# Optimization experiments

Measured on AMD Instinct MI355X. Metric: run time of the kernel, lower is better.

## Reference

```python
import jax, jax.numpy as jnp
import numpy as np
import math

B, N, D, H = 32, 512, 512, 8
DK = D // H
MAX_DIST = 100.0
BINS = 20
BIN_SIZE = MAX_DIST / BINS


def setup_inputs() -> dict:
    key = jax.random.key(0)
    ks = jax.random.split(key, 12)
    s = 1.0 / math.sqrt(D)
    inp = {
        "x": jax.random.normal(ks[0], (B, N, D), dtype=jnp.float32),
        "distance_matrix": jax.random.uniform(ks[1], (B, N, N), dtype=jnp.float32) * MAX_DIST,
        "Wq": jax.random.uniform(ks[2], (D, D), jnp.float32, -s, s),
        "bq": jax.random.uniform(ks[3], (D,), jnp.float32, -s, s),
        "Wk": jax.random.uniform(ks[4], (D, D), jnp.float32, -s, s),
        "bk": jax.random.uniform(ks[5], (D,), jnp.float32, -s, s),
        "Wv": jax.random.uniform(ks[6], (D, D), jnp.float32, -s, s),
        "bv": jax.random.uniform(ks[7], (D,), jnp.float32, -s, s),
        "Wo": jax.random.uniform(ks[8], (D, D), jnp.float32, -s, s),
        "bo": jax.random.uniform(ks[9], (D,), jnp.float32, -s, s),
        "dist_weights": jnp.ones((BINS + 1,), dtype=jnp.float32),
    }
    return inp


def reference(x, distance_matrix, Wq, bq, Wk, bk, Wv, bv, Wo, bo, dist_weights):
    temperature = 1.0
    # Linear projections; torch nn.Linear computes x @ W.T + b
    q = (x @ Wq.T + bq).reshape(B, N, H, DK).transpose(0, 2, 1, 3)  # [B,H,N,DK]
    k = (x @ Wk.T + bk).reshape(B, N, H, DK).transpose(0, 2, 1, 3)
    v = (x @ Wv.T + bv).reshape(B, N, H, DK).transpose(0, 2, 1, 3)

    scores = jnp.einsum("bhqd,bhkd->bhqk", q, k) / math.sqrt(DK)  # [B,H,N,N]

    # Relative position bias: bin distances, look up scalar weight per pair
    binned = jnp.clip((distance_matrix / BIN_SIZE).astype(jnp.int32), 0, BINS)  # [B,N,N]
    bias = dist_weights[binned] / temperature  # [B,N,N]
    scores = scores + bias[:, None, :, :]  # broadcast over heads

    attn = jax.nn.softmax(scores, axis=-1)  # dropout is identity in eval
    out = jnp.einsum("bhqk,bhkd->bhqd", attn, v)  # [B,H,N,DK]
    out = out.transpose(0, 2, 1, 3).reshape(B, N, D)
    return out @ Wo.T + bo
```

## Files before the change

kernel.cpp:

```cpp
#include <hip/hip_runtime.h>
#include <hip/hip_fp16.h>
#include <math.h>
#include <stdint.h>

#define BB 32
#define NN 512
#define DDIM 512
#define HH 8
#define DK 64

typedef __attribute__((ext_vector_type(8))) short short8;
typedef __attribute__((ext_vector_type(8))) _Float16 half8;
typedef __attribute__((ext_vector_type(4))) float floatx4;
typedef __attribute__((ext_vector_type(16))) float floatx16;
typedef unsigned short ushort_t;
typedef unsigned int uint_t;

__device__ __forceinline__ void gl_lds16(const void* g, void* l) {
    __builtin_amdgcn_global_load_lds(
        (const __attribute__((address_space(1))) uint_t*)g,
        (__attribute__((address_space(3))) uint_t*)l,
        16, 0, 0);
}

__device__ __forceinline__ ushort_t f2bf(float f) {
    uint_t u = __builtin_bit_cast(uint_t, f);
    u += 0x7fff + ((u >> 16) & 1);
    return (ushort_t)(u >> 16);
}

__device__ __forceinline__ uint_t pkbf(float a, float b) {
    return (uint_t)f2bf(a) | ((uint_t)f2bf(b) << 16);
}

__device__ __forceinline__ uint_t pkh(float a, float b) {
    return __builtin_bit_cast(uint_t, __builtin_amdgcn_cvt_pkrtz(a, b));
}

__device__ __forceinline__ float h2f(ushort_t u) {
    return __half2float(__ushort_as_half(u));
}

__global__ __launch_bounds__(256) void prep_all(
    const float* __restrict__ x, const float* __restrict__ dist,
    const float* __restrict__ dw,
    const float* __restrict__ Wq, const float* __restrict__ Wk,
    const float* __restrict__ Wv, const float* __restrict__ Wo,
    ushort_t* __restrict__ xb, ushort_t* __restrict__ Tm,
    ushort_t* __restrict__ wqb, ushort_t* __restrict__ wkb,
    ushort_t* __restrict__ wvb, ushort_t* __restrict__ wob) {
    const int bx = blockIdx.x;
    if (bx < 4096) {
        const int i = bx * 256 + threadIdx.x;
        const float4 a = ((const float4*)x)[i * 2 + 0];
        const float4 b = ((const float4*)x)[i * 2 + 1];
        uint4 o;
        o.x = pkbf(a.x, a.y); o.y = pkbf(a.z, a.w);
        o.z = pkbf(b.x, b.y); o.w = pkbf(b.z, b.w);
        *(uint4*)(xb + (size_t)i * 8) = o;
    } else if (bx < 8192) {
        __shared__ float dws[21];
        if (threadIdx.x < 21) dws[threadIdx.x] = (dw[threadIdx.x] - 3.0f) * 1.44269504f;
        __syncthreads();
        const int i = (bx - 4096) * 256 + threadIdx.x;
        float dv[8];
        { const float4 a = ((const float4*)dist)[i * 2 + 0];
          const float4 b = ((const float4*)dist)[i * 2 + 1];
          dv[0]=a.x; dv[1]=a.y; dv[2]=a.z; dv[3]=a.w;
          dv[4]=b.x; dv[5]=b.y; dv[6]=b.z; dv[7]=b.w; }
        ushort_t h[8];
        #pragma unroll
        for (int j = 0; j < 8; ++j) {
            int bin = (int)(dv[j] / 5.0f);
            bin = bin < 0 ? 0 : (bin > 20 ? 20 : bin);
            h[j] = __half_as_ushort(__float2half(dws[bin]));
        }
        uint4 o;
        o.x = (uint_t)h[0] | ((uint_t)h[1] << 16);
        o.y = (uint_t)h[2] | ((uint_t)h[3] << 16);
        o.z = (uint_t)h[4] | ((uint_t)h[5] << 16);
        o.w = (uint_t)h[6] | ((uint_t)h[7] << 16);
        *(uint4*)(Tm + (size_t)i * 8) = o;
    } else {
        const int bw = bx - 8192;
        const int w = bw >> 7;
        const float* s; ushort_t* d;
        if (w == 0)      { s = Wq; d = wqb; }
        else if (w == 1) { s = Wk; d = wkb; }
        else if (w == 2) { s = Wv; d = wvb; }
        else             { s = Wo; d = wob; }
        const int i = (bw & 127) * 256 + threadIdx.x;
        const float4 a = ((const float4*)s)[i * 2 + 0];
        const float4 b = ((const float4*)s)[i * 2 + 1];
        uint4 o;
        o.x = pkbf(a.x, a.y); o.y = pkbf(a.z, a.w);
        o.z = pkbf(b.x, b.y); o.w = pkbf(b.z, b.w);
        *(uint4*)(d + (size_t)i * 8) = o;
    }
}

#define GEMM_CORE(Aptr, Wptr, M0, N0)                                                   \
    __shared__ ushort_t SH[2][128 * 32];                                                \
    ushort_t* const As = SH[0];                                                         \
    ushort_t* const Bs = SH[1];                                                         \
    const int tid = threadIdx.x;                                                        \
    const int lane = tid & 63, wid = tid >> 6;                                          \
    const int quad = lane >> 4, l15 = lane & 15;                                        \
    const int m0 = (M0), n0 = (N0);                                                     \
    const int wy = wid >> 1, wx = wid & 1;                                              \
    floatx4 acc[4][4];                                                                  \
    _Pragma("unroll") for (int i = 0; i < 4; ++i)                                       \
        _Pragma("unroll") for (int j = 0; j < 4; ++j)                                   \
            _Pragma("unroll") for (int r = 0; r < 4; ++r) acc[i][j][r] = 0.f;           \
    for (int k0 = 0; k0 < DDIM; k0 += 32) {                                             \
        __syncthreads();                                                                \
        _Pragma("unroll") for (int j = 0; j < 4; ++j) {                                 \
            const int t = wid * 4 + j;                                                  \
            const int rowi = ((t & 7) << 4) + (lane >> 2);                              \
            const int cd = (lane & 3) ^ ((rowi >> 1) & 3);                              \
            if (t < 8)                                                                  \
                gl_lds16(Aptr + (size_t)(m0 + rowi) * DDIM + k0 + cd * 8,               \
                         (char*)As + ((t & 7) << 10));                                  \
            else                                                                        \
                gl_lds16(Wptr + (size_t)(n0 + rowi) * DDIM + k0 + cd * 8,               \
                         (char*)Bs + ((t & 7) << 10));                                  \
        }                                                                               \
        __syncthreads();                                                                \
        short8 aw[4], bt[4];                                                            \
        _Pragma("unroll") for (int fi = 0; fi < 4; ++fi) {                              \
            const int r = wy * 64 + fi * 16 + l15;                                      \
            aw[fi] = *(const short8*)((const char*)Bs + r * 64 +                        \
                                      ((quad ^ ((r >> 1) & 3)) << 4));                  \
        }                                                                               \
        _Pragma("unroll") for (int ti = 0; ti < 4; ++ti) {                              \
            const int r = wx * 64 + ti * 16 + l15;                                      \
            bt[ti] = *(const short8*)((const char*)As + r * 64 +                        \
                                      ((quad ^ ((r >> 1) & 3)) << 4));                  \
        }                                                                               \
        _Pragma("unroll") for (int fi = 0; fi < 4; ++fi)                                \
            _Pragma("unroll") for (int ti = 0; ti < 4; ++ti)                            \
                acc[fi][ti] = __builtin_amdgcn_mfma_f32_16x16x32_bf16(                  \
                    aw[fi], bt[ti], acc[fi][ti], 0, 0, 0);                              \
    }

__global__ __launch_bounds__(256)
__attribute__((amdgpu_waves_per_eu(2, 2)))
void gemm_qkv(
    const ushort_t* __restrict__ A,
    const ushort_t* __restrict__ W0, const ushort_t* __restrict__ W1,
    const ushort_t* __restrict__ W2,
    const float* __restrict__ b0, const float* __restrict__ b1,
    const float* __restrict__ b2,
    ushort_t* __restrict__ o0, ushort_t* __restrict__ o1, ushort_t* __restrict__ o2) {
    __shared__ ushort_t SH[4][128 * 32];
    const int tid = threadIdx.x;
    const int lane = tid & 63, wid = tid >> 6;
    const int quad = lane >> 4, l15 = lane & 15;
    const int m0 = blockIdx.x * 128, n0 = blockIdx.y * 128;
    const int wy = wid >> 1, wx = wid & 1;

    floatx4 acc[3][4][4];
    #pragma unroll
    for (int w = 0; w < 3; ++w)
        #pragma unroll
        for (int i = 0; i < 4; ++i)
            #pragma unroll
            for (int j = 0; j < 4; ++j)
                #pragma unroll
                for (int r = 0; r < 4; ++r) acc[w][i][j][r] = 0.f;

    const ushort_t* const stage_src =
        (wid == 0) ? A : (wid == 1 ? W0 : (wid == 2 ? W1 : W2));
    const int stage_base = (wid == 0) ? m0 : n0;

    for (int k0 = 0; k0 < DDIM; k0 += 32) {
        __syncthreads();
        #pragma unroll
        for (int j = 0; j < 8; ++j) {
            const int rowi = (j << 4) + (lane >> 2);
            const int cd = (lane & 3) ^ ((rowi >> 1) & 3);
            gl_lds16(stage_src + (size_t)(stage_base + rowi) * DDIM + k0 + cd * 8,
                     (char*)&SH[wid][0] + (j << 10));
        }
        __syncthreads();
        short8 bt[4];
        #pragma unroll
        for (int ti = 0; ti < 4; ++ti) {
            const int r = wx * 64 + ti * 16 + l15;
            bt[ti] = *(const short8*)((const char*)&SH[0][0] + r * 64 +
                                      ((quad ^ ((r >> 1) & 3)) << 4));
        }
        #pragma unroll
        for (int w = 0; w < 3; ++w) {
            short8 aw[4];
            #pragma unroll
            for (int fi = 0; fi < 4; ++fi) {
                const int r = wy * 64 + fi * 16 + l15;
                aw[fi] = *(const short8*)((const char*)&SH[1 + w][0] + r * 64 +
                                          ((quad ^ ((r >> 1) & 3)) << 4));
            }
            #pragma unroll
            for (int fi = 0; fi < 4; ++fi)
                #pragma unroll
                for (int ti = 0; ti < 4; ++ti)
                    acc[w][fi][ti] = __builtin_amdgcn_mfma_f32_16x16x32_bf16(
                        aw[fi], bt[ti], acc[w][fi][ti], 0, 0, 0);
        }
    }

    #pragma unroll
    for (int w = 0; w < 2; ++w) {
        const float* const bias = w ? b1 : b0;
        ushort_t* const dst = w ? o1 : o0;
        #pragma unroll
        for (int fi = 0; fi < 4; ++fi) {
            const int f = n0 + wy * 64 + fi * 16 + quad * 4;
            const float4 b4 = *(const float4*)&bias[f];
            #pragma unroll
            for (int ti = 0; ti < 4; ++ti) {
                const int token = m0 + wx * 64 + ti * 16 + l15;
                const float v0 = acc[w][fi][ti][0] + b4.x, v1 = acc[w][fi][ti][1] + b4.y;
                const float v2 = acc[w][fi][ti][2] + b4.z, v3 = acc[w][fi][ti][3] + b4.w;
                uint2 v;
                v.x = pkbf(v0, v1); v.y = pkbf(v2, v3);
                *(uint2*)&dst[(size_t)token * DDIM + f] = v;
            }
        }
    }

    {
        const int b = m0 >> 9;
        const int hh0 = n0 >> 6;
        ushort_t* const SHT = &SH[0][0];
        __syncthreads();
        #pragma unroll
        for (int hp = 0; hp < 2; ++hp) {
            if (wy == hp) {
                #pragma unroll
                for (int fi = 0; fi < 4; ++fi) {
                    const int f = n0 + wy * 64 + fi * 16 + quad * 4;
                    const float4 b4 = *(const float4*)&b2[f];
                    #pragma unroll
                    for (int ti = 0; ti < 4; ++ti) {
                        const int q = wx * 64 + ti * 16 + l15;
                        const int qc = q >> 3, qr = q & 7;
                        const float vv[4] = {acc[2][fi][ti][0] + b4.x,
                                             acc[2][fi][ti][1] + b4.y,
                                             acc[2][fi][ti][2] + b4.z,
                                             acc[2][fi][ti][3] + b4.w};
                        #pragma unroll
                        for (int r = 0; r < 4; ++r) {
                            const int d = fi * 16 + quad * 4 + r;
                            SHT[(d * 256 + ((qc ^ (d & 15)) << 4) + qr * 2) >> 1] =
                                __half_as_ushort(__float2half(vv[r]));
                        }
                    }
                }
            }
            __syncthreads();
            const size_t vbase = ((size_t)(b * HH + hh0 + hp)) * DK;
            #pragma unroll
            for (int c = 0; c < 4; ++c) {
                const int ch = tid + 256 * c;
                const int d = ch >> 4, chl = ch & 15;
                const uint4 vv = *(const uint4*)((const char*)SHT + d * 256 +
                                                 ((chl ^ (d & 15)) << 4));
                *(uint4*)&o2[(vbase + d) * NN + (m0 & 511) + chl * 8] = vv;
            }
            __syncthreads();
        }
    }
}

__global__ __launch_bounds__(256) void gemm_out(
    const ushort_t* __restrict__ A, const ushort_t* __restrict__ Wo,
    const float* __restrict__ bo, float* __restrict__ dst) {
    GEMM_CORE(A, Wo, blockIdx.x * 128, blockIdx.y * 128)
    #pragma unroll
    for (int fi = 0; fi < 4; ++fi) {
        const int f = n0 + wy * 64 + fi * 16 + quad * 4;
        const float4 b4 = *(const float4*)&bo[f];
        #pragma unroll
        for (int ti = 0; ti < 4; ++ti) {
            const int token = m0 + wx * 64 + ti * 16 + l15;
            float4 v;
            v.x = acc[fi][ti][0] + b4.x; v.y = acc[fi][ti][1] + b4.y;
            v.z = acc[fi][ti][2] + b4.z; v.w = acc[fi][ti][3] + b4.w;
            *(float4*)&dst[(size_t)token * DDIM + f] = v;
        }
    }
}

__global__ __launch_bounds__(512)
__attribute__((amdgpu_waves_per_eu(2, 2)))
void attn_fused(
    const ushort_t* __restrict__ Qg, const ushort_t* __restrict__ Kg,
    const ushort_t* __restrict__ Vtg, const ushort_t* __restrict__ Tg,
    ushort_t* __restrict__ aout) {
    __shared__ ushort_t Ks[512 * 64];
    __shared__ ushort_t Vs[64 * 512];

    const int tid = threadIdx.x, lane = tid & 63, wid = tid >> 6;
    const int l31 = lane & 31, hl = lane >> 5;
    const int p = blockIdx.x;
    const int nid = (p & 7) * 32 + (p >> 3);
    const int h = nid & 7, b = nid >> 3;
    const float K1 = 0.18033688f;

    #pragma unroll
    for (int j = 0; j < 8; ++j) {
        const int t = wid * 8 + j;
        {
            const int row = t * 8 + (lane >> 3);
            const int key = (row & 7) ^ ((row >> 3) & 7);
            const int g = (lane & 7) ^ key;
            gl_lds16(Kg + (size_t)(b * NN + row) * DDIM + h * DK + g * 8,
                     (char*)Ks + t * 1024);
        }
        {
            const int key = (t & 7) ^ ((t >> 3) & 7);
            const int g = lane ^ key;
            gl_lds16(Vtg + (size_t)((b * HH + h) * DK + t) * NN + g * 8,
                     (char*)Vs + t * 1024);
        }
    }

    short8 bq[2][4];
    #pragma unroll
    for (int qt = 0; qt < 2; ++qt) {
        const ushort_t* qp =
            Qg + (size_t)(b * NN + wid * 64 + qt * 32 + l31) * DDIM + h * DK + hl * 8;
        #pragma unroll
        for (int st = 0; st < 4; ++st) bq[qt][st] = *(const short8*)(qp + st * 16);
    }

    float lsum[2] = {0.f, 0.f};
    floatx16 O[2][2];
    #pragma unroll
    for (int qt = 0; qt < 2; ++qt)
        #pragma unroll
        for (int dt = 0; dt < 2; ++dt)
            #pragma unroll
            for (int r = 0; r < 16; ++r) O[qt][dt][r] = 0.f;

    __syncthreads();

    for (int kt = 0; kt < 8; ++kt) {
        uint2 tv[2][2][4];
        #pragma unroll
        for (int qt = 0; qt < 2; ++qt) {
            const ushort_t* tp =
                Tg + (size_t)(b * NN + wid * 64 + qt * 32 + l31) * NN + kt * 64 + hl * 4;
            #pragma unroll
            for (int kti = 0; kti < 2; ++kti)
                #pragma unroll
                for (int g = 0; g < 4; ++g)
                    tv[qt][kti][g] = *(const uint2*)(tp + kti * 32 + g * 8);
        }

        #pragma unroll
        for (int kti = 0; kti < 2; ++kti) {
            short8 kf[4];
            {
                const int row = kt * 64 + kti * 32 + l31;
                const int key = (row & 7) ^ ((row >> 3) & 7);
                #pragma unroll
                for (int st = 0; st < 4; ++st)
                    kf[st] = *(const short8*)((const char*)Ks + row * 128 +
                                              (((st * 2 + hl) ^ key) << 4));
            }
            half8 vf[2][2];
            #pragma unroll
            for (int dt = 0; dt < 2; ++dt) {
                const int d = dt * 32 + l31;
                const int key = (d & 7) ^ ((d >> 3) & 7);
                #pragma unroll
                for (int ks = 0; ks < 2; ++ks)
                    vf[dt][ks] = *(const half8*)((const char*)Vs + d * 1024 +
                        (((kt * 8 + kti * 4 + ks * 2 + hl) ^ key) << 4));
            }

            #pragma unroll
            for (int qt = 0; qt < 2; ++qt) {
                floatx16 S;
                #pragma unroll
                for (int r = 0; r < 16; ++r) S[r] = 0.f;
                __builtin_amdgcn_s_setprio(1);
                #pragma unroll
                for (int st = 0; st < 4; ++st)
                    S = __builtin_amdgcn_mfma_f32_32x32x16_bf16(
                        kf[st], bq[qt][st], S, 0, 0, 0);
                __builtin_amdgcn_s_setprio(0);

                float ls = 0.f;
                #pragma unroll
                for (int ks = 0; ks < 2; ++ks) {
                    float pp[8];
                    #pragma unroll
                    for (int gg = 0; gg < 2; ++gg) {
                        const uint2 tg = tv[qt][kti][ks * 2 + gg];
                        const float t0 = h2f((ushort_t)tg.x);
                        const float t1 = h2f((ushort_t)(tg.x >> 16));
                        const float t2 = h2f((ushort_t)tg.y);
                        const float t3 = h2f((ushort_t)(tg.y >> 16));
                        const int sb = ks * 8 + gg * 4;
                        pp[gg * 4 + 0] = exp2f(S[sb + 0] * K1 + t0);
                        pp[gg * 4 + 1] = exp2f(S[sb + 1] * K1 + t1);
                        pp[gg * 4 + 2] = exp2f(S[sb + 2] * K1 + t2);
                        pp[gg * 4 + 3] = exp2f(S[sb + 3] * K1 + t3);
                        ls += (pp[gg * 4 + 0] + pp[gg * 4 + 1]) +
                              (pp[gg * 4 + 2] + pp[gg * 4 + 3]);
                    }
                    uint_t w0 = pkh(pp[0], pp[1]);
                    uint_t w1 = pkh(pp[2], pp[3]);
                    uint_t w2 = pkh(pp[4], pp[5]);
                    uint_t w3 = pkh(pp[6], pp[7]);
                    auto r02 = __builtin_amdgcn_permlane32_swap(w0, w2, false, false);
                    auto r13 = __builtin_amdgcn_permlane32_swap(w1, w3, false, false);
                    uint4 uu;
                    uu.x = r02[0];
                    uu.y = r13[0];
                    uu.z = r02[1];
                    uu.w = r13[1];
                    const half8 bp = __builtin_bit_cast(half8, uu);

                    __builtin_amdgcn_s_setprio(1);
                    #pragma unroll
                    for (int dt = 0; dt < 2; ++dt)
                        O[qt][dt] = __builtin_amdgcn_mfma_f32_32x32x16_f16(
                            vf[dt][ks], bp, O[qt][dt], 0, 0, 0);
                    __builtin_amdgcn_s_setprio(0);
                }
                lsum[qt] += ls;
            }
        }
    }

    #pragma unroll
    for (int qt = 0; qt < 2; ++qt) {
        float l = lsum[qt];
        l += __shfl_xor(l, 32);
        const float inv = 1.0f / l;
        const size_t orow =
            (size_t)(b * NN + wid * 64 + qt * 32 + l31) * DDIM + h * DK;
        #pragma unroll
        for (int dt = 0; dt < 2; ++dt)
            #pragma unroll
            for (int g = 0; g < 4; ++g) {
                const int d = dt * 32 + g * 8 + hl * 4;
                uint2 ov;
                ov.x = pkbf(O[qt][dt][g * 4 + 0] * inv, O[qt][dt][g * 4 + 1] * inv);
                ov.y = pkbf(O[qt][dt][g * 4 + 2] * inv, O[qt][dt][g * 4 + 3] * inv);
                *(uint2*)&aout[orow + d] = ov;
            }
    }
}

extern "C" void kernel_launch(void* const* d_in, const int* in_sizes, int n_in,
                              void* d_out, int out_size, void* d_ws, size_t ws_size,
                              hipStream_t stream) {
    const float* x    = (const float*)d_in[0];
    const float* dist = (const float*)d_in[1];
    const float* Wq   = (const float*)d_in[2];
    const float* bq   = (const float*)d_in[3];
    const float* Wk   = (const float*)d_in[4];
    const float* bk   = (const float*)d_in[5];
    const float* Wv   = (const float*)d_in[6];
    const float* bv   = (const float*)d_in[7];
    const float* Wo   = (const float*)d_in[8];
    const float* bo   = (const float*)d_in[9];
    const float* dw   = (const float*)d_in[10];
    float* out = (float*)d_out;

    const size_t NELT = (size_t)BB * NN * DDIM;
    ushort_t* xb  = (ushort_t*)d_ws;
    ushort_t* wqb = xb + NELT;
    ushort_t* wkb = wqb + DDIM * DDIM;
    ushort_t* wvb = wkb + DDIM * DDIM;
    ushort_t* wob = wvb + DDIM * DDIM;
    ushort_t* qb  = wob + DDIM * DDIM;
    ushort_t* kb  = qb + NELT;
    ushort_t* vt  = kb + NELT;
    ushort_t* Tm  = vt + NELT;
    ushort_t* ab  = xb;

    prep_all<<<8704, 256, 0, stream>>>(x, dist, dw, Wq, Wk, Wv, Wo,
                                       xb, Tm, wqb, wkb, wvb, wob);
    gemm_qkv<<<dim3(128, 4), 256, 0, stream>>>(xb, wqb, wkb, wvb, bq, bk, bv,
                                               qb, kb, vt);
    attn_fused<<<256, 512, 0, stream>>>(qb, kb, vt, Tm, ab);
    gemm_out<<<dim3(128, 4), 256, 0, stream>>>(ab, wob, bo, out);
}
```

Before: 224.9 us.

## Split attention blocks over query halves, read V fragments from global in MFMA layout

The attention kernel now launches twice as many blocks, each handling half the query rows of a (batch, head), with one 32-row query tile per wave instead of two. The V tile is no longer staged in LDS. The QKV GEMM now writes V^T in a 16-query chunked layout so each lane can load its MFMA fragment straight from global/L2, and the occupancy hint rises to 4 waves per EU. This is meant to cut LDS use and per-block register pressure to raise occupancy on the 256 CUs. In exchange, V is re-read from L2 by every wave and K is loaded into LDS twice per (batch, head).

```diff
diff --git a/kernel.cpp b/kernel.cpp
--- a/kernel.cpp
+++ b/kernel.cpp
@@ -231,6 +231,7 @@
     {
         const int b = m0 >> 9;
         const int hh0 = n0 >> 6;
+        const int q0 = m0 & 511;
         ushort_t* const SHT = &SH[0][0];
         __syncthreads();
         #pragma unroll
@@ -258,14 +259,15 @@
                 }
             }
             __syncthreads();
-            const size_t vbase = ((size_t)(b * HH + hh0 + hp)) * DK;
+            const size_t slab = (size_t)(b * HH + hh0 + hp) * DK * NN;
             #pragma unroll
             for (int c = 0; c < 4; ++c) {
-                const int ch = tid + 256 * c;
-                const int d = ch >> 4, chl = ch & 15;
+                const int idx = c * 256 + tid;
+                const int d = (idx >> 1) & 63, hf = idx & 1, qc2 = idx >> 7;
+                const int qchl = qc2 * 2 + hf;
                 const uint4 vv = *(const uint4*)((const char*)SHT + d * 256 +
-                                                 ((chl ^ (d & 15)) << 4));
-                *(uint4*)&o2[(vbase + d) * NN + (m0 & 511) + chl * 8] = vv;
+                                                 ((qchl ^ (d & 15)) << 4));
+                *(uint4*)&o2[slab + (size_t)((q0 >> 4) + qc2) * 1024 + d * 16 + hf * 8] = vv;
             }
             __syncthreads();
         }
@@ -292,74 +294,73 @@
 }
 
 __global__ __launch_bounds__(512)
-__attribute__((amdgpu_waves_per_eu(2, 2)))
+__attribute__((amdgpu_waves_per_eu(4, 4)))
 void attn_fused(
     const ushort_t* __restrict__ Qg, const ushort_t* __restrict__ Kg,
     const ushort_t* __restrict__ Vtg, const ushort_t* __restrict__ Tg,
     ushort_t* __restrict__ aout) {
     __shared__ ushort_t Ks[512 * 64];
-    __shared__ ushort_t Vs[64 * 512];
 
     const int tid = threadIdx.x, lane = tid & 63, wid = tid >> 6;
     const int l31 = lane & 31, hl = lane >> 5;
     const int p = blockIdx.x;
-    const int nid = (p & 7) * 32 + (p >> 3);
-    const int h = nid & 7, b = nid >> 3;
+    const int nid = (p & 7) * 64 + (p >> 3);
+    const int h = nid & 7, b = (nid >> 3) & 31, qh = nid >> 8;
+    const int qbase = qh * 256 + wid * 32;
     const float K1 = 0.18033688f;
 
     #pragma unroll
     for (int j = 0; j < 8; ++j) {
         const int t = wid * 8 + j;
+        const int row = t * 8 + (lane >> 3);
+        const int key = (row & 7) ^ ((row >> 3) & 7);
+        const int g = (lane & 7) ^ key;
+        gl_lds16(Kg + (size_t)(b * NN + row) * DDIM + h * DK + g * 8,
+                 (char*)Ks + t * 1024);
+    }
+
+    short8 bq[4];
+    {
+        const ushort_t* qp =
+            Qg + (size_t)(b * NN + qbase + l31) * DDIM + h * DK + hl * 8;
+        #pragma unroll
+        for (int st = 0; st < 4; ++st) bq[st] = *(const short8*)(qp + st * 16);
+    }
+
+    const ushort_t* const vslab = Vtg + (size_t)(b * HH + h) * DK * NN;
+
+    float lsum = 0.f;
+    floatx16 O[2];
+    #pragma unroll
+    for (int dt = 0; dt < 2; ++dt)
+        #pragma unroll
+        for (int r = 0; r < 16; ++r) O[dt][r] = 0.f;
+
+    __syncthreads();
+
+    for (int kt = 0; kt < 8; ++kt) {
+        uint2 tv[2][4];
         {
-            const int row = t * 8 + (lane >> 3);
-            const int key = (row & 7) ^ ((row >> 3) & 7);
-            const int g = (lane & 7) ^ key;
-            gl_lds16(Kg + (size_t)(b * NN + row) * DDIM + h * DK + g * 8,
-                     (char*)Ks + t * 1024);
-        }
-        {
-            const int key = (t & 7) ^ ((t >> 3) & 7);
-            const int g = lane ^ key;
-            gl_lds16(Vtg + (size_t)((b * HH + h) * DK + t) * NN + g * 8,
-                     (char*)Vs + t * 1024);
-        }
-    }
-
-    short8 bq[2][4];
-    #pragma unroll
-    for (int qt = 0; qt < 2; ++qt) {
-        const ushort_t* qp =
-            Qg + (size_t)(b * NN + wid * 64 + qt * 32 + l31) * DDIM + h * DK + hl * 8;
-        #pragma unroll
-        for (int st = 0; st < 4; ++st) bq[qt][st] = *(const short8*)(qp + st * 16);
-    }
-
-    float lsum[2] = {0.f, 0.f};
-    floatx16 O[2][2];
-    #pragma unroll
-    for (int qt = 0; qt < 2; ++qt)
-        #pragma unroll
-        for (int dt = 0; dt < 2; ++dt)
-            #pragma unroll
-            for (int r = 0; r < 16; ++r) O[qt][dt][r] = 0.f;
-
-    __syncthreads();
-
-    for (int kt = 0; kt < 8; ++kt) {
-        uint2 tv[2][2][4];
-        #pragma unroll
-        for (int qt = 0; qt < 2; ++qt) {
             const ushort_t* tp =
-                Tg + (size_t)(b * NN + wid * 64 + qt * 32 + l31) * NN + kt * 64 + hl * 4;
+                Tg + (size_t)(b * NN + qbase + l31) * NN + kt * 64 + hl * 4;
             #pragma unroll
             for (int kti = 0; kti < 2; ++kti)
                 #pragma unroll
                 for (int g = 0; g < 4; ++g)
-                    tv[qt][kti][g] = *(const uint2*)(tp + kti * 32 + g * 8);
+                    tv[kti][g] = *(const uint2*)(tp + kti * 32 + g * 8);
         }
 
         #pragma unroll
         for (int kti = 0; kti < 2; ++kti) {
+            half8 vf[2][2];
+            #pragma unroll
+            for (int dt = 0; dt < 2; ++dt) {
+                const int d = dt * 32 + l31;
+                #pragma unroll
+                for (int ks = 0; ks < 2; ++ks)
+                    vf[dt][ks] = *(const half8*)&vslab[
+                        (size_t)(kt * 4 + kti * 2 + ks) * 1024 + d * 16 + hl * 8];
+            }
             short8 kf[4];
             {
                 const int row = kt * 64 + kti * 32 + l31;
@@ -369,88 +370,74 @@
                     kf[st] = *(const short8*)((const char*)Ks + row * 128 +
                                               (((st * 2 + hl) ^ key) << 4));
             }
-            half8 vf[2][2];
-            #pragma unroll
-            for (int dt = 0; dt < 2; ++dt) {
-                const int d = dt * 32 + l31;
-                const int key = (d & 7) ^ ((d >> 3) & 7);
-                #pragma unroll
-                for (int ks = 0; ks < 2; ++ks)
-                    vf[dt][ks] = *(const half8*)((const char*)Vs + d * 1024 +
-                        (((kt * 8 + kti * 4 + ks * 2 + hl) ^ key) << 4));
-            }
-
-            #pragma unroll
-            for (int qt = 0; qt < 2; ++qt) {
-                floatx16 S;
-                #pragma unroll
-                for (int r = 0; r < 16; ++r) S[r] = 0.f;
+
+            floatx16 S;
+            #pragma unroll
+            for (int r = 0; r < 16; ++r) S[r] = 0.f;
+            __builtin_amdgcn_s_setprio(1);
+            #pragma unroll
+            for (int st = 0; st < 4; ++st)
+                S = __builtin_amdgcn_mfma_f32_32x32x16_bf16(
+                    kf[st], bq[st], S, 0, 0, 0);
+            __builtin_amdgcn_s_setprio(0);
+
+            float ls = 0.f;
+            #pragma unroll
+            for (int ks = 0; ks < 2; ++ks) {
+                float pp[8];
+                #pragma unroll
+                for (int gg = 0; gg < 2; ++gg) {
+                    const uint2 tg = tv[kti][ks * 2 + gg];
+                    const float t0 = h2f((ushort_t)tg.x);
+                    const float t1 = h2f((ushort_t)(tg.x >> 16));
+                    const float t2 = h2f((ushort_t)tg.y);
+                    const float t3 = h2f((ushort_t)(tg.y >> 16));
+                    const int sb = ks * 8 + gg * 4;
+                    pp[gg * 4 + 0] = exp2f(S[sb + 0] * K1 + t0);
+                    pp[gg * 4 + 1] = exp2f(S[sb + 1] * K1 + t1);
+                    pp[gg * 4 + 2] = exp2f(S[sb + 2] * K1 + t2);
+                    pp[gg * 4 + 3] = exp2f(S[sb + 3] * K1 + t3);
+                    ls += (pp[gg * 4 + 0] + pp[gg * 4 + 1]) +
+                          (pp[gg * 4 + 2] + pp[gg * 4 + 3]);
+                }
+                uint_t w0 = pkh(pp[0], pp[1]);
+                uint_t w1 = pkh(pp[2], pp[3]);
+                uint_t w2 = pkh(pp[4], pp[5]);
+                uint_t w3 = pkh(pp[6], pp[7]);
+                auto r02 = __builtin_amdgcn_permlane32_swap(w0, w2, false, false);
+                auto r13 = __builtin_amdgcn_permlane32_swap(w1, w3, false, false);
+                uint4 uu;
+                uu.x = r02[0];
+                uu.y = r13[0];
+                uu.z = r02[1];
+                uu.w = r13[1];
+                const half8 bp = __builtin_bit_cast(half8, uu);
+
                 __builtin_amdgcn_s_setprio(1);
                 #pragma unroll
-                for (int st = 0; st < 4; ++st)
-                    S = __builtin_amdgcn_mfma_f32_32x32x16_bf16(
-                        kf[st], bq[qt][st], S, 0, 0, 0);
+                for (int dt = 0; dt < 2; ++dt)
+                    O[dt] = __builtin_amdgcn_mfma_f32_32x32x16_f16(
+                        vf[dt][ks], bp, O[dt], 0, 0, 0);
                 __builtin_amdgcn_s_setprio(0);
-
-                float ls = 0.f;
-                #pragma unroll
-                for (int ks = 0; ks < 2; ++ks) {
-                    float pp[8];
-                    #pragma unroll
-                    for (int gg = 0; gg < 2; ++gg) {
-                        const uint2 tg = tv[qt][kti][ks * 2 + gg];
-                        const float t0 = h2f((ushort_t)tg.x);
-                        const float t1 = h2f((ushort_t)(tg.x >> 16));
-                        const float t2 = h2f((ushort_t)tg.y);
-                        const float t3 = h2f((ushort_t)(tg.y >> 16));
-                        const int sb = ks * 8 + gg * 4;
-                        pp[gg * 4 + 0] = exp2f(S[sb + 0] * K1 + t0);
-                        pp[gg * 4 + 1] = exp2f(S[sb + 1] * K1 + t1);
-                        pp[gg * 4 + 2] = exp2f(S[sb + 2] * K1 + t2);
-                        pp[gg * 4 + 3] = exp2f(S[sb + 3] * K1 + t3);
-                        ls += (pp[gg * 4 + 0] + pp[gg * 4 + 1]) +
-                              (pp[gg * 4 + 2] + pp[gg * 4 + 3]);
-                    }
-                    uint_t w0 = pkh(pp[0], pp[1]);
-                    uint_t w1 = pkh(pp[2], pp[3]);
-                    uint_t w2 = pkh(pp[4], pp[5]);
-                    uint_t w3 = pkh(pp[6], pp[7]);
-                    auto r02 = __builtin_amdgcn_permlane32_swap(w0, w2, false, false);
-                    auto r13 = __builtin_amdgcn_permlane32_swap(w1, w3, false, false);
-                    uint4 uu;
-                    uu.x = r02[0];
-                    uu.y = r13[0];
-                    uu.z = r02[1];
-                    uu.w = r13[1];
-                    const half8 bp = __builtin_bit_cast(half8, uu);
-
-                    __builtin_amdgcn_s_setprio(1);
-                    #pragma unroll
-                    for (int dt = 0; dt < 2; ++dt)
-                        O[qt][dt] = __builtin_amdgcn_mfma_f32_32x32x16_f16(
-                            vf[dt][ks], bp, O[qt][dt], 0, 0, 0);
-                    __builtin_amdgcn_s_setprio(0);
-                }
-                lsum[qt] += ls;
-            }
-        }
-    }
-
-    #pragma unroll
-    for (int qt = 0; qt < 2; ++qt) {
-        float l = lsum[qt];
+            }
+            lsum += ls;
+        }
+    }
+
+    {
+        float l = lsum;
         l += __shfl_xor(l, 32);
         const float inv = 1.0f / l;
         const size_t orow =
-            (size_t)(b * NN + wid * 64 + qt * 32 + l31) * DDIM + h * DK;
+            (size_t)(b * NN + qbase + l31) * DDIM + h * DK;
         #pragma unroll
         for (int dt = 0; dt < 2; ++dt)
             #pragma unroll
             for (int g = 0; g < 4; ++g) {
                 const int d = dt * 32 + g * 8 + hl * 4;
                 uint2 ov;
-                ov.x = pkbf(O[qt][dt][g * 4 + 0] * inv, O[qt][dt][g * 4 + 1] * inv);
-                ov.y = pkbf(O[qt][dt][g * 4 + 2] * inv, O[qt][dt][g * 4 + 3] * inv);
+                ov.x = pkbf(O[dt][g * 4 + 0] * inv, O[dt][g * 4 + 1] * inv);
+                ov.y = pkbf(O[dt][g * 4 + 2] * inv, O[dt][g * 4 + 3] * inv);
                 *(uint2*)&aout[orow + d] = ov;
             }
     }
@@ -488,6 +475,6 @@
                                        xb, Tm, wqb, wkb, wvb, wob);
     gemm_qkv<<<dim3(128, 4), 256, 0, stream>>>(xb, wqb, wkb, wvb, bq, bk, bv,
                                                qb, kb, vt);
-    attn_fused<<<256, 512, 0, stream>>>(qb, kb, vt, Tm, ab);
+    attn_fused<<<512, 512, 0, stream>>>(qb, kb, vt, Tm, ab);
     gemm_out<<<dim3(128, 4), 256, 0, stream>>>(ab, wob, bo, out);
 }
```

New measurement: 239.5 us. 6.5% more time.
